# Kernel tuning notes

Measured on AMD Instinct MI355X. Metric: run time of the kernel, lower is better.

The kernel has to match this reference:

```python
import jax, jax.numpy as jnp
import numpy as np

N_CLASSES = 80
SEG_LEN = 512          # boxes per class (uniform segments)
H = 128                # hidden_size
DH = 2 * H             # decoder hidden (= concat of bidirectional encoder final hiddens)
EMB = 32               # decoder_input_dim
SOS, EOS = 2, 3


def _gru_cell(x, h, Wih, Whh, bih, bhh):
    # PyTorch GRU cell math. x:(in,), h:(hid,), Wih:(3*hid,in), Whh:(3*hid,hid)
    gi = Wih @ x + bih
    gh = Whh @ h + bhh
    i_r, i_z, i_n = jnp.split(gi, 3)
    h_r, h_z, h_n = jnp.split(gh, 3)
    r = jax.nn.sigmoid(i_r + h_r)
    z = jax.nn.sigmoid(i_z + h_z)
    n = jnp.tanh(i_n + r * h_n)
    return (1.0 - z) * n + z * h


def _gru_seq(xs, h0, Wih, Whh, bih, bhh):
    # xs: (T, in); returns final hidden (hid,) and all hiddens (T, hid)
    def step(h, x):
        h2 = _gru_cell(x, h, Wih, Whh, bih, bhh)
        return h2, h2
    hT, hs = jax.lax.scan(step, h0, xs)
    return hT, hs

# vmap over the 80 classes (per-class weights)
_run_gru = jax.vmap(_gru_seq, in_axes=(0, 0, 0, 0, 0, 0))


def setup_inputs() -> dict:
    key = jax.random.key(0)
    ks = jax.random.split(key, 32)
    N = N_CLASSES * SEG_LEN
    s = 0.05
    inp = {
        "feat": jax.random.normal(ks[0], (N, 1024), jnp.float32),
        "score": jax.random.uniform(ks[1], (N, 1), jnp.float32),
        "box": jax.random.uniform(ks[2], (N, 4), jnp.float32),
        "origin_score": jax.random.uniform(ks[3], (N, 91), jnp.float32),
        "labels": jax.random.randint(ks[4], (N,), 0, 2, jnp.int64),
        "weights": jax.random.uniform(ks[5], (N,), jnp.float32),
        "unique_class": jnp.ones((N_CLASSES,), jnp.int64),
        "unique_class_len": jnp.arange(N_CLASSES + 1, dtype=jnp.int64) * SEG_LEN,
        # shared linears
        "appear_W": jax.random.normal(ks[6], (H, 1024), jnp.float32) * s,
        "appear_b": jnp.zeros((H,), jnp.float32),
        "featlin_W": jax.random.normal(ks[7], (H, H + 96), jnp.float32) * s,
        "featlin_b": jnp.zeros((H,), jnp.float32),
        # per-class bidirectional encoder GRUs
        "enc_Wih_f": jax.random.normal(ks[8], (N_CLASSES, 3 * H, H), jnp.float32) * s,
        "enc_Whh_f": jax.random.normal(ks[9], (N_CLASSES, 3 * H, H), jnp.float32) * s,
        "enc_bih_f": jnp.zeros((N_CLASSES, 3 * H), jnp.float32),
        "enc_bhh_f": jnp.zeros((N_CLASSES, 3 * H), jnp.float32),
        "enc_Wih_b": jax.random.normal(ks[10], (N_CLASSES, 3 * H, H), jnp.float32) * s,
        "enc_Whh_b": jax.random.normal(ks[11], (N_CLASSES, 3 * H, H), jnp.float32) * s,
        "enc_bih_b": jnp.zeros((N_CLASSES, 3 * H), jnp.float32),
        "enc_bhh_b": jnp.zeros((N_CLASSES, 3 * H), jnp.float32),
        # decoder
        "dec_emb": jax.random.normal(ks[12], (4, EMB), jnp.float32) * s,
        "dec_Wih": jax.random.normal(ks[13], (N_CLASSES, 3 * DH, EMB), jnp.float32) * s,
        "dec_Whh": jax.random.normal(ks[14], (N_CLASSES, 3 * DH, DH), jnp.float32) * s,
        "dec_bih": jnp.zeros((N_CLASSES, 3 * DH), jnp.float32),
        "dec_bhh": jnp.zeros((N_CLASSES, 3 * DH), jnp.float32),
        "out_W": jax.random.normal(ks[15], (4, DH), jnp.float32) * s,
        "out_b": jnp.zeros((4,), jnp.float32),
    }
    return inp


def reference(feat, score, box, origin_score, labels, weights, unique_class,
              unique_class_len, appear_W, appear_b, featlin_W, featlin_b,
              enc_Wih_f, enc_Whh_f, enc_bih_f, enc_bhh_f,
              enc_Wih_b, enc_Whh_b, enc_bih_b, enc_bhh_b,
              dec_emb, dec_Wih, dec_Whh, dec_bih, dec_bhh, out_W, out_b):
    # --- shared feature encoding ---
    x = jax.nn.relu(feat @ appear_W.T + appear_b)                    # (N, H)
    allf = jnp.concatenate([x, score, box, origin_score], axis=1)    # (N, H+96)
    enc_feat = jax.nn.relu(allf @ featlin_W.T + featlin_b)           # (N, H)

    # --- per-class bidirectional encoder (uniform segments) ---
    seg = enc_feat.reshape(N_CLASSES, SEG_LEN, H)
    eos = jnp.ones((N_CLASSES, 1, H), enc_feat.dtype)                # encoder_EOS = ones
    enc_in = jnp.concatenate([seg, eos], axis=1)                     # (80, L+1, H)
    h0 = jnp.zeros((N_CLASSES, H), enc_feat.dtype)
    h_f, _ = _run_gru(enc_in, h0, enc_Wih_f, enc_Whh_f, enc_bih_f, enc_bhh_f)
    h_b, _ = _run_gru(enc_in[:, ::-1], h0, enc_Wih_b, enc_Whh_b, enc_bih_b, enc_bhh_b)
    dec_h0 = jnp.concatenate([h_f, h_b], axis=-1)                    # (80, 2H)

    # --- per-class decoder with teacher forcing (SOS then gold labels) ---
    emb = dec_emb[labels].reshape(N_CLASSES, SEG_LEN, EMB)
    sos = jnp.broadcast_to(dec_emb[SOS], (N_CLASSES, 1, EMB))
    dec_in = jnp.concatenate([sos, emb], axis=1)                     # (80, L+1, EMB)
    _, dec_hs = _run_gru(dec_in, dec_h0, dec_Wih, dec_Whh, dec_bih, dec_bhh)

    logits = dec_hs.reshape(-1, DH) @ out_W.T + out_b                # (80*(L+1), 4)
    output = jax.nn.log_softmax(logits, axis=-1)
    return output, labels, weights
```

## Files before the change

kernel.cpp:

```cpp
#include <hip/hip_runtime.h>


typedef __fp16 h2v __attribute__((ext_vector_type(2)));

__device__ __forceinline__ h2v pk2(float a, float b) {
  return __builtin_amdgcn_cvt_pkrtz(a, b);
}
__device__ __forceinline__ unsigned h2u(h2v h) { return __builtin_bit_cast(unsigned, h); }
__device__ __forceinline__ h2v u2h(unsigned u) { return __builtin_bit_cast(h2v, u); }
__device__ __forceinline__ float fdot2f(h2v a, h2v b, float c) {
  return __builtin_amdgcn_fdot2(a, b, c, false);
}
__device__ __forceinline__ float sigf(float x) { return 1.f / (1.f + __expf(-x)); }
__device__ __forceinline__ float tanhfast(float x) { return 2.f / (1.f + __expf(-2.f * x)) - 1.f; }

__device__ __forceinline__ uint4 pack8u(float4 a, float4 b) {
  uint4 o;
  o.x = h2u(pk2(a.x, a.y)); o.y = h2u(pk2(a.z, a.w));
  o.z = h2u(pk2(b.x, b.y)); o.w = h2u(pk2(b.z, b.w));
  return o;
}

__device__ __forceinline__ float dotu4(uint4 cv, h2v a0, h2v a1, h2v a2, h2v a3,
                                       float acc) {
  acc = fdot2f(u2h(cv.x), a0, acc);
  acc = fdot2f(u2h(cv.y), a1, acc);
  acc = fdot2f(u2h(cv.z), a2, acc);
  acc = fdot2f(u2h(cv.w), a3, acc);
  return acc;
}

template <int CTRL>
__device__ __forceinline__ float dppadd(float acc, float v) {
  int r = __builtin_amdgcn_update_dpp(0, __float_as_int(v), CTRL, 0xF, 0xF, true);
  return acc + __int_as_float(r);
}
__device__ __forceinline__ float swz4add(float acc, float v) {
  return acc + __int_as_float(__builtin_amdgcn_ds_swizzle(__float_as_int(v), 0x101F));
}

__device__ __forceinline__ float reduce8s(float p0, float p1, float p2, float p3,
                                          float p4, float p5, float p6, float p7) {
  p0 = dppadd<0xB1>(p0, p1);
  p2 = dppadd<0xB1>(p2, p3);
  p4 = dppadd<0xB1>(p4, p5);
  p6 = dppadd<0xB1>(p6, p7);
  p0 = dppadd<0x4E>(p0, p2);
  p4 = dppadd<0x4E>(p4, p6);
  p0 = swz4add(p0, p4);
  p0 = dppadd<0x128>(p0, p0);
  return p0;
}

#define BAR_LGKM()                                     \
  asm volatile("s_waitcnt lgkmcnt(0)" ::: "memory");   \
  __builtin_amdgcn_s_barrier();                        \
  asm volatile("" ::: "memory");

__global__ void k_fill_misc(const float* __restrict__ score, const float* __restrict__ box,
                            const float* __restrict__ orig, float* __restrict__ allf) {
  int i = blockIdx.x * blockDim.x + threadIdx.x;
  if (i >= 40960 * 96) return;
  int row = i / 96, k = i - row * 96;
  float v;
  if (k == 0) v = score[row];
  else if (k < 5) v = box[row * 4 + (k - 1)];
  else v = orig[(size_t)row * 91 + (k - 5)];
  allf[(size_t)row * 224 + 128 + k] = v;
}

__global__ __launch_bounds__(256) void k_gemm_appear(
    const float* __restrict__ A, const float* __restrict__ W,
    const float* __restrict__ bias, float* __restrict__ allf) {
  __shared__ float As[32][68];
  __shared__ float Ws[32][132];
  const int tid = threadIdx.x;
  const int tx = tid & 15, ty = tid >> 4;
  const int r0 = blockIdx.x * 64;
  const int lr = tid >> 3;
  const int lk = (tid & 7) * 4;
  float acc[4][8];
#pragma unroll
  for (int i = 0; i < 4; ++i)
#pragma unroll
    for (int j = 0; j < 8; ++j) acc[i][j] = 0.f;

  for (int k0 = 0; k0 < 1024; k0 += 32) {
#pragma unroll
    for (int i = 0; i < 2; ++i) {
      int rr = lr + i * 32;
      float4 v = *(const float4*)(A + (size_t)(r0 + rr) * 1024 + k0 + lk);
      As[lk + 0][rr] = v.x; As[lk + 1][rr] = v.y; As[lk + 2][rr] = v.z; As[lk + 3][rr] = v.w;
    }
#pragma unroll
    for (int i = 0; i < 4; ++i) {
      int wr = lr + i * 32;
      float4 v = *(const float4*)(W + (size_t)wr * 1024 + k0 + lk);
      Ws[lk + 0][wr] = v.x; Ws[lk + 1][wr] = v.y; Ws[lk + 2][wr] = v.z; Ws[lk + 3][wr] = v.w;
    }
    __syncthreads();
#pragma unroll
    for (int kk = 0; kk < 32; ++kk) {
      float4 a = *(const float4*)&As[kk][ty * 4];
      float4 w0 = *(const float4*)&Ws[kk][tx * 8];
      float4 w1 = *(const float4*)&Ws[kk][tx * 8 + 4];
      float av[4] = {a.x, a.y, a.z, a.w};
      float wv[8] = {w0.x, w0.y, w0.z, w0.w, w1.x, w1.y, w1.z, w1.w};
#pragma unroll
      for (int i = 0; i < 4; ++i)
#pragma unroll
        for (int j = 0; j < 8; ++j) acc[i][j] = fmaf(av[i], wv[j], acc[i][j]);
    }
    __syncthreads();
  }
#pragma unroll
  for (int i = 0; i < 4; ++i) {
    int row = r0 + ty * 4 + i;
#pragma unroll
    for (int j = 0; j < 8; ++j) {
      int col = tx * 8 + j;
      float v = acc[i][j] + bias[col];
      allf[(size_t)row * 224 + col] = fmaxf(v, 0.f);
    }
  }
}

__global__ __launch_bounds__(256) void k_gemm_featlin(
    const float* __restrict__ A, const float* __restrict__ W,
    const float* __restrict__ bias, unsigned* __restrict__ encf2) {
  __shared__ float As[32][68];
  __shared__ float Ws[32][132];
  const int tid = threadIdx.x;
  const int tx = tid & 15, ty = tid >> 4;
  const int r0 = blockIdx.x * 64;
  const int lr = tid >> 3;
  const int lk = (tid & 7) * 4;
  float acc[4][8];
#pragma unroll
  for (int i = 0; i < 4; ++i)
#pragma unroll
    for (int j = 0; j < 8; ++j) acc[i][j] = 0.f;

  for (int k0 = 0; k0 < 224; k0 += 32) {
#pragma unroll
    for (int i = 0; i < 2; ++i) {
      int rr = lr + i * 32;
      float4 v = *(const float4*)(A + (size_t)(r0 + rr) * 224 + k0 + lk);
      As[lk + 0][rr] = v.x; As[lk + 1][rr] = v.y; As[lk + 2][rr] = v.z; As[lk + 3][rr] = v.w;
    }
#pragma unroll
    for (int i = 0; i < 4; ++i) {
      int wr = lr + i * 32;
      float4 v = *(const float4*)(W + (size_t)wr * 224 + k0 + lk);
      Ws[lk + 0][wr] = v.x; Ws[lk + 1][wr] = v.y; Ws[lk + 2][wr] = v.z; Ws[lk + 3][wr] = v.w;
    }
    __syncthreads();
#pragma unroll
    for (int kk = 0; kk < 32; ++kk) {
      float4 a = *(const float4*)&As[kk][ty * 4];
      float4 w0 = *(const float4*)&Ws[kk][tx * 8];
      float4 w1 = *(const float4*)&Ws[kk][tx * 8 + 4];
      float av[4] = {a.x, a.y, a.z, a.w};
      float wv[8] = {w0.x, w0.y, w0.z, w0.w, w1.x, w1.y, w1.z, w1.w};
#pragma unroll
      for (int i = 0; i < 4; ++i)
#pragma unroll
        for (int j = 0; j < 8; ++j) acc[i][j] = fmaf(av[i], wv[j], acc[i][j]);
    }
    __syncthreads();
  }
#pragma unroll
  for (int i = 0; i < 4; ++i) {
    int row = r0 + ty * 4 + i;
    unsigned* orow = encf2 + (size_t)row * 64;
#pragma unroll
    for (int p = 0; p < 4; ++p) {
      int col = tx * 8 + 2 * p;
      float a = fmaxf(acc[i][2 * p] + bias[col], 0.f);
      float b = fmaxf(acc[i][2 * p + 1] + bias[col + 1], 0.f);
      orow[tx * 4 + p] = h2u(pk2(a, b));
    }
  }
}

__global__ __launch_bounds__(256) void k_dec_gi(
    const float* __restrict__ Wih, const float* __restrict__ bih,
    const float* __restrict__ emb, float* __restrict__ gi) {
  __shared__ float e[4][32];
  const int c = blockIdx.x, tid = threadIdx.x;
  if (tid < 128) e[tid >> 5][tid & 31] = emb[tid];
  __syncthreads();
#pragma unroll
  for (int i = 0; i < 3; ++i) {
    int r = tid + i * 256;
    const float* w = Wih + ((size_t)c * 768 + r) * 32;
    float b = bih[(size_t)c * 768 + r];
    float a0 = b, a1 = b, a2 = b, a3 = b;
#pragma unroll
    for (int k = 0; k < 32; ++k) {
      float wv = w[k];
      a0 = fmaf(wv, e[0][k], a0);
      a1 = fmaf(wv, e[1][k], a1);
      a2 = fmaf(wv, e[2][k], a2);
      a3 = fmaf(wv, e[3][k], a3);
    }
    gi[((size_t)c * 4 + 0) * 768 + r] = a0;
    gi[((size_t)c * 4 + 1) * 768 + r] = a1;
    gi[((size_t)c * 4 + 2) * 768 + r] = a2;
    gi[((size_t)c * 4 + 3) * 768 + r] = a3;
  }
}

__global__ __launch_bounds__(512) void k_pack_dec(
    const float* __restrict__ Whh, uint4* __restrict__ wpk) {
  const int c = blockIdx.x / 48, ic = blockIdx.x % 48;
  const int tid = threadIdx.x;
  const int G = tid >> 4, m = tid & 15, mw = m & 7;
  const int gt = ic >> 4, k = (ic & 15) >> 1, hf = ic & 1;
  const int row = gt * 256 + 8 * G + (k ^ mw);
  const float* src = Whh + ((size_t)c * 768 + row) * 256 + 16 * m + 8 * hf;
  wpk[((size_t)c * 48 + ic) * 512 + tid] =
      pack8u(*(const float4*)src, *(const float4*)(src + 4));
}

#define ELOAD(gt, k, DST)                                                          \
  {                                                                                \
    int rid_ = (k) ^ mw;                                                           \
    const float* Mx_ = ((k) & 1) ? baseB : baseA;                                  \
    const float4* ps_ =                                                            \
        (const float4*)(Mx_ + ((size_t)((gt) * 128 + 4 * G + (rid_ >> 1))) * 128 + \
                        8 * m);                                                    \
    DST = pack8u(ps_[0], ps_[1]);                                                  \
  }                                                                                \
  __builtin_amdgcn_sched_barrier(0);

__global__ __launch_bounds__(512) void k_enc_gru(
    const unsigned* __restrict__ encf2,
    const float* __restrict__ WihF, const float* __restrict__ WhhF,
    const float* __restrict__ bihF, const float* __restrict__ bhhF,
    const float* __restrict__ WihB, const float* __restrict__ WhhB,
    const float* __restrict__ bihB, const float* __restrict__ bhhB,
    float* __restrict__ dec_h0) {
  const int blk = blockIdx.x;
  const int c = blk >> 1, dir = blk & 1;
  const int tid = threadIdx.x;
  const int G = tid >> 4, m = tid & 15, mw = m & 7;

  const float* Wih = (dir ? WihB : WihF) + (size_t)c * 384 * 128;
  const float* Whh = (dir ? WhhB : WhhF) + (size_t)c * 384 * 128;
  const float* bih = (dir ? bihB : bihF) + (size_t)c * 384;
  const float* bhh = (dir ? bhhB : bhhF) + (size_t)c * 384;

  const float* baseA = (mw & 1) ? Whh : Wih;
  const float* baseB = (mw & 1) ? Wih : Whh;

  __shared__ __align__(16) unsigned x2s[2][64];
  __shared__ __align__(16) unsigned h2s[2][64];
  __shared__ __align__(16) uint4 wle[8 * 512];

  uint4 er0, er1, er2, er3, er4, er5, er6, er7;
  uint4 ez0, ez1, ez2, ez3, ez4, ez5, ez6, ez7;
  ELOAD(0, 0, er0) ELOAD(0, 1, er1) ELOAD(0, 2, er2) ELOAD(0, 3, er3)
  ELOAD(0, 4, er4) ELOAD(0, 5, er5) ELOAD(0, 6, er6) ELOAD(0, 7, er7)
  ELOAD(1, 0, ez0) ELOAD(1, 1, ez1) ELOAD(1, 2, ez2) ELOAD(1, 3, ez3)
  ELOAD(1, 4, ez4) ELOAD(1, 5, ez5) ELOAD(1, 6, ez6) ELOAD(1, 7, ez7)
  {
    uint4 t0;
    ELOAD(2, 0, t0) wle[0 * 512 + tid] = t0;
    ELOAD(2, 1, t0) wle[1 * 512 + tid] = t0;
    ELOAD(2, 2, t0) wle[2 * 512 + tid] = t0;
    ELOAD(2, 3, t0) wle[3 * 512 + tid] = t0;
    ELOAD(2, 4, t0) wle[4 * 512 + tid] = t0;
    ELOAD(2, 5, t0) wle[5 * 512 + tid] = t0;
    ELOAD(2, 6, t0) wle[6 * 512 + tid] = t0;
    ELOAD(2, 7, t0) wle[7 * 512 + tid] = t0;
  }

  const int u = 4 * G + (mw >> 1);
  const float brz_r = bih[u] + bhh[u];
  const float brz_z = bih[128 + u] + bhh[128 + u];
  const float b_in = bih[256 + u];
  const float b_hn = bhh[256 + u];

  if (tid < 64) h2s[0][tid] = 0u;
  if (tid >= 448) {
    int lane = tid - 448;
    x2s[0][lane] = (dir == 0) ? encf2[((size_t)c * 512 + 0) * 64 + lane] : 0x3C003C00u;
  }
  float hreg = 0.f;
  __syncthreads();

  const uint4* wl = wle + tid;

  for (int t = 0; t <= 512; ++t) {
    unsigned xpre = 0;
    if (tid >= 448 && t < 512) {
      int tn = t + 1, lane = tid - 448;
      int row = (dir == 0) ? ((tn < 512) ? tn : -1) : (512 - tn);
      xpre = (row < 0) ? 0x3C003C00u : encf2[((size_t)c * 512 + row) * 64 + lane];
    }
    uint4 xv = ((const uint4*)&x2s[t & 1][0])[m];
    uint4 hv = ((const uint4*)&h2s[t & 1][0])[m];
    h2v x0 = u2h(xv.x), x1 = u2h(xv.y), x2 = u2h(xv.z), x3 = u2h(xv.w);
    h2v hh0 = u2h(hv.x), hh1 = u2h(hv.y), hh2 = u2h(hv.z), hh3 = u2h(hv.w);
    bool oddl = (mw & 1);
    h2v a0 = oddl ? hh0 : x0, a1 = oddl ? hh1 : x1, a2 = oddl ? hh2 : x2, a3 = oddl ? hh3 : x3;
    h2v b0 = oddl ? x0 : hh0, b1 = oddl ? x1 : hh1, b2 = oddl ? x2 : hh2, b3 = oddl ? x3 : hh3;
#define EA(ch) dotu4(ch, a0, a1, a2, a3, 0.f)
#define EB(ch) dotu4(ch, b0, b1, b2, b3, 0.f)
    float vR = reduce8s(EA(er0), EB(er1), EA(er2), EB(er3),
                        EA(er4), EB(er5), EA(er6), EB(er7));
    float vZ = reduce8s(EA(ez0), EB(ez1), EA(ez2), EB(ez3),
                        EA(ez4), EB(ez5), EA(ez6), EB(ez7));
    float vN = reduce8s(EA(wl[0 * 512]), EB(wl[1 * 512]), EA(wl[2 * 512]), EB(wl[3 * 512]),
                        EA(wl[4 * 512]), EB(wl[5 * 512]), EA(wl[6 * 512]), EB(wl[7 * 512]));
#undef EA
#undef EB
    float oR = __shfl_xor(vR, 1, 64);
    float oZ = __shfl_xor(vZ, 1, 64);
    float oN = __shfl_xor(vN, 1, 64);
    float r = sigf(vR + oR + brz_r);
    float z = sigf(vZ + oZ + brz_z);
    float i_n = oddl ? oN : vN;
    float h_n = oddl ? vN : oN;
    float n = tanhfast(i_n + b_in + r * (h_n + b_hn));
    float hn = (1.f - z) * n + z * hreg;
    hreg = hn;
    float prt = __shfl_xor(hn, 2, 64);
    if (m < 8 && (mw & 3) == 0) h2s[(t + 1) & 1][2 * G + (mw >> 2)] = h2u(pk2(hn, prt));
    if (tid >= 448 && t < 512) x2s[(t + 1) & 1][tid - 448] = xpre;
    BAR_LGKM();
  }
  if ((m < 8) && ((mw & 1) == 0))
    dec_h0[(size_t)c * 256 + dir * 128 + u] = hreg;
}

#define CONSX(sa, sb) dotu4(sb, g4, g5, g6, g7, dotu4(sa, g0, g1, g2, g3, 0.f))

__global__ __launch_bounds__(512) void k_dec_gru(
    const uint4* __restrict__ wpk, const float* __restrict__ bhh,
    const float* __restrict__ gi, const float* __restrict__ h0,
    const int* __restrict__ labels, unsigned* __restrict__ dhs2) {
  const int c = blockIdx.x, tid = threadIdx.x;
  const int G = tid >> 4, m = tid & 15, mw = m & 7;

  __shared__ __align__(16) unsigned h2s[2][128];
  __shared__ int labs[513];
  __shared__ __align__(16) uint4 wlds[12 * 512];

  const uint4* wp = wpk + (size_t)c * 48 * 512 + tid;
  const uint4* wpS = wp + 36 * 512;

  for (int j = 0; j < 12; ++j) wlds[j * 512 + tid] = wp[(24 + j) * 512];
  __builtin_amdgcn_sched_barrier(0);
  uint4 ra0 = wp[0 * 512], ra1 = wp[1 * 512], ra2 = wp[2 * 512], ra3 = wp[3 * 512];
  uint4 ra4 = wp[4 * 512], ra5 = wp[5 * 512], ra6 = wp[6 * 512], ra7 = wp[7 * 512];
  __builtin_amdgcn_sched_barrier(0);
  uint4 ra8 = wp[8 * 512], ra9 = wp[9 * 512], ra10 = wp[10 * 512], ra11 = wp[11 * 512];
  uint4 ra12 = wp[12 * 512], ra13 = wp[13 * 512], ra14 = wp[14 * 512], ra15 = wp[15 * 512];
  __builtin_amdgcn_sched_barrier(0);
  uint4 ra16 = wp[16 * 512], ra17 = wp[17 * 512], ra18 = wp[18 * 512], ra19 = wp[19 * 512];
  uint4 ra20 = wp[20 * 512], ra21 = wp[21 * 512], ra22 = wp[22 * 512], ra23 = wp[23 * 512];
  __builtin_amdgcn_sched_barrier(0);
  uint4 ss0 = wpS[0 * 512], ss1 = wpS[1 * 512], ss2 = wpS[2 * 512], ss3 = wpS[3 * 512];
  uint4 ss4 = wpS[4 * 512], ss5 = wpS[5 * 512], ss6 = wpS[6 * 512], ss7 = wpS[7 * 512];
  uint4 ss8 = wpS[8 * 512], ss9 = wpS[9 * 512], ss10 = wpS[10 * 512], ss11 = wpS[11 * 512];

  const int u = 8 * G + mw;
  const float bb0 = bhh[(size_t)c * 768 + u];
  const float bb1 = bhh[(size_t)c * 768 + 256 + u];
  const float bb2 = bhh[(size_t)c * 768 + 512 + u];
  const float* gib = gi + (size_t)c * 4 * 768;
  unsigned* dout = dhs2 + (size_t)c * 513 * 128 + 4 * G + (mw >> 1);

  if (tid < 512) labs[tid + 1] = labels[(size_t)c * 512 + tid];
  if (tid == 0) labs[0] = 2;
  float hreg = h0[(size_t)c * 256 + u];
  {
    float oth = __shfl_xor(hreg, 1, 64);
    if (m < 8 && (mw & 1) == 0) h2s[0][4 * G + (mw >> 1)] = h2u(pk2(hreg, oth));
  }
  __syncthreads();

  const uint4* wl = wlds + tid;

  for (int t = 0; t <= 512; ++t) {
    uint4 ha = ((const uint4*)&h2s[t & 1][0])[2 * m];
    uint4 hb = ((const uint4*)&h2s[t & 1][0])[2 * m + 1];
    h2v g0 = u2h(ha.x), g1 = u2h(ha.y), g2 = u2h(ha.z), g3 = u2h(ha.w);
    h2v g4 = u2h(hb.x), g5 = u2h(hb.y), g6 = u2h(hb.z), g7 = u2h(hb.w);
    int sel = labs[t];
    const float* gp = gib + sel * 768;
    float giR = gp[u], giZ = gp[256 + u], giN = gp[512 + u];
    float p0 = CONSX(ra0, ra1), p1 = CONSX(ra2, ra3);
    float p2 = CONSX(ra4, ra5), p3 = CONSX(ra6, ra7);
    float p4 = CONSX(ra8, ra9), p5 = CONSX(ra10, ra11);
    float p6 = CONSX(ra12, ra13), p7 = CONSX(ra14, ra15);
    float rsum = reduce8s(p0, p1, p2, p3, p4, p5, p6, p7);
    p0 = CONSX(ra16, ra17); p1 = CONSX(ra18, ra19);
    p2 = CONSX(ra20, ra21); p3 = CONSX(ra22, ra23);
    p4 = CONSX(wl[0 * 512], wl[1 * 512]);
    p5 = CONSX(wl[2 * 512], wl[3 * 512]);
    p6 = CONSX(wl[4 * 512], wl[5 * 512]);
    p7 = CONSX(wl[6 * 512], wl[7 * 512]);
    float zsum = reduce8s(p0, p1, p2, p3, p4, p5, p6, p7);
    p0 = CONSX(wl[8 * 512], wl[9 * 512]);
    p1 = CONSX(wl[10 * 512], wl[11 * 512]);
    p2 = CONSX(ss0, ss1); ss0 = wpS[0 * 512]; ss1 = wpS[1 * 512];
    p3 = CONSX(ss2, ss3); ss2 = wpS[2 * 512]; ss3 = wpS[3 * 512];
    p4 = CONSX(ss4, ss5); ss4 = wpS[4 * 512]; ss5 = wpS[5 * 512];
    p5 = CONSX(ss6, ss7); ss6 = wpS[6 * 512]; ss7 = wpS[7 * 512];
    p6 = CONSX(ss8, ss9); ss8 = wpS[8 * 512]; ss9 = wpS[9 * 512];
    p7 = CONSX(ss10, ss11); ss10 = wpS[10 * 512]; ss11 = wpS[11 * 512];
    float nsum = reduce8s(p0, p1, p2, p3, p4, p5, p6, p7);
    float r = sigf(giR + rsum + bb0);
    float z = sigf(giZ + zsum + bb1);
    float n = tanhfast(giN + r * (nsum + bb2));
    float hn = (1.f - z) * n + z * hreg;
    hreg = hn;
    float oth = __shfl_xor(hn, 1, 64);
    if (m < 8 && (mw & 1) == 0) {
      unsigned pk = h2u(pk2(hn, oth));
      h2s[(t + 1) & 1][4 * G + (mw >> 1)] = pk;
      dout[(size_t)t * 128] = pk;
    }
    BAR_LGKM();
  }
}

__global__ __launch_bounds__(256) void k_out(
    const unsigned* __restrict__ dhs2, const float* __restrict__ outW,
    const float* __restrict__ outB, float* __restrict__ out) {
  int row = blockIdx.x * 4 + (threadIdx.x >> 6);
  if (row >= 41040) return;
  int lane = threadIdx.x & 63;
  const unsigned* hp = dhs2 + (size_t)row * 128 + 2 * lane;
  h2v ha = u2h(hp[0]), hb = u2h(hp[1]);
  float h0f = (float)ha[0], h1f = (float)ha[1], h2f = (float)hb[0], h3f = (float)hb[1];
  float p0, p1, p2, p3;
  {
    const float* w0 = outW + 4 * lane;
    const float* w1 = outW + 256 + 4 * lane;
    const float* w2 = outW + 512 + 4 * lane;
    const float* w3 = outW + 768 + 4 * lane;
    p0 = h0f * w0[0] + h1f * w0[1] + h2f * w0[2] + h3f * w0[3];
    p1 = h0f * w1[0] + h1f * w1[1] + h2f * w1[2] + h3f * w1[3];
    p2 = h0f * w2[0] + h1f * w2[1] + h2f * w2[2] + h3f * w2[3];
    p3 = h0f * w3[0] + h1f * w3[1] + h2f * w3[2] + h3f * w3[3];
  }
#pragma unroll
  for (int off = 32; off > 0; off >>= 1) {
    p0 += __shfl_xor(p0, off, 64);
    p1 += __shfl_xor(p1, off, 64);
    p2 += __shfl_xor(p2, off, 64);
    p3 += __shfl_xor(p3, off, 64);
  }
  if (lane == 0) {
    float l0 = p0 + outB[0], l1 = p1 + outB[1], l2 = p2 + outB[2], l3 = p3 + outB[3];
    float mm = fmaxf(fmaxf(l0, l1), fmaxf(l2, l3));
    float s = __expf(l0 - mm) + __expf(l1 - mm) + __expf(l2 - mm) + __expf(l3 - mm);
    float lse = mm + __logf(s);
    float* o = out + (size_t)row * 4;
    o[0] = l0 - lse; o[1] = l1 - lse; o[2] = l2 - lse; o[3] = l3 - lse;
  }
}

__global__ void k_passthrough(const int* __restrict__ labels,
                              const float* __restrict__ weights,
                              float* __restrict__ out) {
  int i = blockIdx.x * blockDim.x + threadIdx.x;
  if (i < 40960) {
    out[164160 + i] = (float)labels[i];
    out[164160 + 40960 + i] = weights[i];
  }
}

extern "C" void kernel_launch(void* const* d_in, const int* in_sizes, int n_in,
                              void* d_out, int out_size, void* d_ws, size_t ws_size,
                              hipStream_t stream) {
  (void)in_sizes; (void)n_in; (void)out_size; (void)ws_size;
  const float* feat = (const float*)d_in[0];
  const float* score = (const float*)d_in[1];
  const float* box = (const float*)d_in[2];
  const float* orig = (const float*)d_in[3];
  const int* labels = (const int*)d_in[4];
  const float* weights = (const float*)d_in[5];
  const float* appear_W = (const float*)d_in[8];
  const float* appear_b = (const float*)d_in[9];
  const float* featlin_W = (const float*)d_in[10];
  const float* featlin_b = (const float*)d_in[11];
  const float* eWihF = (const float*)d_in[12];
  const float* eWhhF = (const float*)d_in[13];
  const float* ebihF = (const float*)d_in[14];
  const float* ebhhF = (const float*)d_in[15];
  const float* eWihB = (const float*)d_in[16];
  const float* eWhhB = (const float*)d_in[17];
  const float* ebihB = (const float*)d_in[18];
  const float* ebhhB = (const float*)d_in[19];
  const float* dec_emb = (const float*)d_in[20];
  const float* dWih = (const float*)d_in[21];
  const float* dWhh = (const float*)d_in[22];
  const float* dbih = (const float*)d_in[23];
  const float* dbhh = (const float*)d_in[24];
  const float* outW = (const float*)d_in[25];
  const float* outB = (const float*)d_in[26];
  float* out = (float*)d_out;

  char* ws = (char*)d_ws;
  float* allf = (float*)ws;
  unsigned* encf2 = (unsigned*)(ws + (size_t)40960 * 224 * 4);
  float* dec_h0 = (float*)(ws + (size_t)40960 * 224 * 4 + (size_t)40960 * 64 * 4);
  float* dec_gi = dec_h0 + 80 * 256;
  unsigned* dhs2 = (unsigned*)(dec_gi + 80 * 4 * 768);
  uint4* wpack = (uint4*)allf;

  k_fill_misc<<<15360, 256, 0, stream>>>(score, box, orig, allf);
  k_gemm_appear<<<640, 256, 0, stream>>>(feat, appear_W, appear_b, allf);
  k_gemm_featlin<<<640, 256, 0, stream>>>(allf, featlin_W, featlin_b, encf2);
  k_pack_dec<<<80 * 48, 512, 0, stream>>>(dWhh, wpack);
  k_dec_gi<<<80, 256, 0, stream>>>(dWih, dbih, dec_emb, dec_gi);
  k_enc_gru<<<160, 512, 0, stream>>>(encf2, eWihF, eWhhF, ebihF, ebhhF,
                                     eWihB, eWhhB, ebihB, ebhhB, dec_h0);
  k_dec_gru<<<80, 512, 0, stream>>>(wpack, dbhh, dec_gi, dec_h0, labels, dhs2);
  k_out<<<10260, 256, 0, stream>>>(dhs2, outW, outB, out);
  k_passthrough<<<160, 256, 0, stream>>>(labels, weights, out);
}
```

Measured before the change: 1.557 ms.

## Split decoder GRU rows across thread pairs with 1024-thread blocks

The decoder GRU kernel now runs 1024 threads per block instead of 512. Each hidden unit's dot product over its K dimension is split between two adjacent lanes, which combine their partial sums with a lane shuffle. The weight packing kernel is reorganised to match this layout. Per-thread register-held and LDS-held weight chunks are roughly halved, which shortens the serial per-step dot-product chain. In exchange it adds an extra shuffle reduction and a larger barrier across 16 waves per step.

```diff
diff --git a/kernel.cpp b/kernel.cpp
--- a/kernel.cpp
+++ b/kernel.cpp
@@ -211,15 +211,17 @@
   }
 }
 
-__global__ __launch_bounds__(512) void k_pack_dec(
+__global__ __launch_bounds__(1024) void k_pack_dec(
     const float* __restrict__ Whh, uint4* __restrict__ wpk) {
-  const int c = blockIdx.x / 48, ic = blockIdx.x % 48;
+  const int c = blockIdx.x / 24, ic = blockIdx.x % 24;
   const int tid = threadIdx.x;
   const int G = tid >> 4, m = tid & 15, mw = m & 7;
-  const int gt = ic >> 4, k = (ic & 15) >> 1, hf = ic & 1;
-  const int row = gt * 256 + 8 * G + (k ^ mw);
+  const int gt = ic >> 3, k = ic & 7;
+  const int rid = k ^ mw;
+  const int row = gt * 256 + 4 * G + (rid >> 1);
+  const int hf = rid & 1;
   const float* src = Whh + ((size_t)c * 768 + row) * 256 + 16 * m + 8 * hf;
-  wpk[((size_t)c * 48 + ic) * 512 + tid] =
+  wpk[((size_t)c * 24 + ic) * 1024 + tid] =
       pack8u(*(const float4*)src, *(const float4*)(src + 4));
 }
 
@@ -335,9 +337,7 @@
     dec_h0[(size_t)c * 256 + dir * 128 + u] = hreg;
 }
 
-#define CONSX(sa, sb) dotu4(sb, g4, g5, g6, g7, dotu4(sa, g0, g1, g2, g3, 0.f))
-
-__global__ __launch_bounds__(512) void k_dec_gru(
+__global__ __launch_bounds__(1024) void k_dec_gru(
     const uint4* __restrict__ wpk, const float* __restrict__ bhh,
     const float* __restrict__ gi, const float* __restrict__ h0,
     const int* __restrict__ labels, unsigned* __restrict__ dhs2) {
@@ -346,39 +346,33 @@
 
   __shared__ __align__(16) unsigned h2s[2][128];
   __shared__ int labs[513];
-  __shared__ __align__(16) uint4 wlds[12 * 512];
-
-  const uint4* wp = wpk + (size_t)c * 48 * 512 + tid;
-  const uint4* wpS = wp + 36 * 512;
-
-  for (int j = 0; j < 12; ++j) wlds[j * 512 + tid] = wp[(24 + j) * 512];
+  __shared__ __align__(16) uint4 wlds[9 * 1024];
+
+  const uint4* wp = wpk + (size_t)c * 24 * 1024 + tid;
+  const uint4* wpS = wp + 21 * 1024;
+
+  for (int j = 0; j < 9; ++j) wlds[j * 1024 + tid] = wp[(12 + j) * 1024];
   __builtin_amdgcn_sched_barrier(0);
-  uint4 ra0 = wp[0 * 512], ra1 = wp[1 * 512], ra2 = wp[2 * 512], ra3 = wp[3 * 512];
-  uint4 ra4 = wp[4 * 512], ra5 = wp[5 * 512], ra6 = wp[6 * 512], ra7 = wp[7 * 512];
+  uint4 rr0 = wp[0 * 1024], rr1 = wp[1 * 1024], rr2 = wp[2 * 1024], rr3 = wp[3 * 1024];
+  uint4 rr4 = wp[4 * 1024], rr5 = wp[5 * 1024], rr6 = wp[6 * 1024], rr7 = wp[7 * 1024];
   __builtin_amdgcn_sched_barrier(0);
-  uint4 ra8 = wp[8 * 512], ra9 = wp[9 * 512], ra10 = wp[10 * 512], ra11 = wp[11 * 512];
-  uint4 ra12 = wp[12 * 512], ra13 = wp[13 * 512], ra14 = wp[14 * 512], ra15 = wp[15 * 512];
+  uint4 rz0 = wp[8 * 1024], rz1 = wp[9 * 1024], rz2 = wp[10 * 1024], rz3 = wp[11 * 1024];
   __builtin_amdgcn_sched_barrier(0);
-  uint4 ra16 = wp[16 * 512], ra17 = wp[17 * 512], ra18 = wp[18 * 512], ra19 = wp[19 * 512];
-  uint4 ra20 = wp[20 * 512], ra21 = wp[21 * 512], ra22 = wp[22 * 512], ra23 = wp[23 * 512];
-  __builtin_amdgcn_sched_barrier(0);
-  uint4 ss0 = wpS[0 * 512], ss1 = wpS[1 * 512], ss2 = wpS[2 * 512], ss3 = wpS[3 * 512];
-  uint4 ss4 = wpS[4 * 512], ss5 = wpS[5 * 512], ss6 = wpS[6 * 512], ss7 = wpS[7 * 512];
-  uint4 ss8 = wpS[8 * 512], ss9 = wpS[9 * 512], ss10 = wpS[10 * 512], ss11 = wpS[11 * 512];
-
-  const int u = 8 * G + mw;
-  const float bb0 = bhh[(size_t)c * 768 + u];
-  const float bb1 = bhh[(size_t)c * 768 + 256 + u];
-  const float bb2 = bhh[(size_t)c * 768 + 512 + u];
+  uint4 ss0 = wpS[0 * 1024], ss1 = wpS[1 * 1024], ss2 = wpS[2 * 1024];
+
+  const int u = 4 * G + (mw >> 1);
+  const float bbR = bhh[(size_t)c * 768 + u];
+  const float bbZ = bhh[(size_t)c * 768 + 256 + u];
+  const float bbN = bhh[(size_t)c * 768 + 512 + u];
   const float* gib = gi + (size_t)c * 4 * 768;
-  unsigned* dout = dhs2 + (size_t)c * 513 * 128 + 4 * G + (mw >> 1);
+  unsigned* dout = dhs2 + (size_t)c * 513 * 128 + 2 * G + (mw >> 2);
 
   if (tid < 512) labs[tid + 1] = labels[(size_t)c * 512 + tid];
   if (tid == 0) labs[0] = 2;
   float hreg = h0[(size_t)c * 256 + u];
   {
-    float oth = __shfl_xor(hreg, 1, 64);
-    if (m < 8 && (mw & 1) == 0) h2s[0][4 * G + (mw >> 1)] = h2u(pk2(hreg, oth));
+    float oth = __shfl_xor(hreg, 2, 64);
+    if (m < 8 && (mw & 3) == 0) h2s[0][2 * G + (mw >> 2)] = h2u(pk2(hreg, oth));
   }
   __syncthreads();
 
@@ -389,39 +383,42 @@
     uint4 hb = ((const uint4*)&h2s[t & 1][0])[2 * m + 1];
     h2v g0 = u2h(ha.x), g1 = u2h(ha.y), g2 = u2h(ha.z), g3 = u2h(ha.w);
     h2v g4 = u2h(hb.x), g5 = u2h(hb.y), g6 = u2h(hb.z), g7 = u2h(hb.w);
+    bool oddl = (mw & 1);
+    h2v ga0 = oddl ? g4 : g0, ga1 = oddl ? g5 : g1, ga2 = oddl ? g6 : g2, ga3 = oddl ? g7 : g3;
+    h2v gb0 = oddl ? g0 : g4, gb1 = oddl ? g1 : g5, gb2 = oddl ? g2 : g6, gb3 = oddl ? g3 : g7;
+#define CA(ch) dotu4(ch, ga0, ga1, ga2, ga3, 0.f)
+#define CB(ch) dotu4(ch, gb0, gb1, gb2, gb3, 0.f)
     int sel = labs[t];
     const float* gp = gib + sel * 768;
     float giR = gp[u], giZ = gp[256 + u], giN = gp[512 + u];
-    float p0 = CONSX(ra0, ra1), p1 = CONSX(ra2, ra3);
-    float p2 = CONSX(ra4, ra5), p3 = CONSX(ra6, ra7);
-    float p4 = CONSX(ra8, ra9), p5 = CONSX(ra10, ra11);
-    float p6 = CONSX(ra12, ra13), p7 = CONSX(ra14, ra15);
-    float rsum = reduce8s(p0, p1, p2, p3, p4, p5, p6, p7);
-    p0 = CONSX(ra16, ra17); p1 = CONSX(ra18, ra19);
-    p2 = CONSX(ra20, ra21); p3 = CONSX(ra22, ra23);
-    p4 = CONSX(wl[0 * 512], wl[1 * 512]);
-    p5 = CONSX(wl[2 * 512], wl[3 * 512]);
-    p6 = CONSX(wl[4 * 512], wl[5 * 512]);
-    p7 = CONSX(wl[6 * 512], wl[7 * 512]);
-    float zsum = reduce8s(p0, p1, p2, p3, p4, p5, p6, p7);
-    p0 = CONSX(wl[8 * 512], wl[9 * 512]);
-    p1 = CONSX(wl[10 * 512], wl[11 * 512]);
-    p2 = CONSX(ss0, ss1); ss0 = wpS[0 * 512]; ss1 = wpS[1 * 512];
-    p3 = CONSX(ss2, ss3); ss2 = wpS[2 * 512]; ss3 = wpS[3 * 512];
-    p4 = CONSX(ss4, ss5); ss4 = wpS[4 * 512]; ss5 = wpS[5 * 512];
-    p5 = CONSX(ss6, ss7); ss6 = wpS[6 * 512]; ss7 = wpS[7 * 512];
-    p6 = CONSX(ss8, ss9); ss8 = wpS[8 * 512]; ss9 = wpS[9 * 512];
-    p7 = CONSX(ss10, ss11); ss10 = wpS[10 * 512]; ss11 = wpS[11 * 512];
-    float nsum = reduce8s(p0, p1, p2, p3, p4, p5, p6, p7);
-    float r = sigf(giR + rsum + bb0);
-    float z = sigf(giZ + zsum + bb1);
-    float n = tanhfast(giN + r * (nsum + bb2));
+    float vR = reduce8s(CA(rr0), CB(rr1), CA(rr2), CB(rr3),
+                        CA(rr4), CB(rr5), CA(rr6), CB(rr7));
+    float vZ = reduce8s(CA(rz0), CB(rz1), CA(rz2), CB(rz3),
+                        CA(wl[0 * 1024]), CB(wl[1 * 1024]),
+                        CA(wl[2 * 1024]), CB(wl[3 * 1024]));
+    float p0 = CA(wl[4 * 1024]);
+    float p1 = CB(wl[5 * 1024]);
+    float p2 = CA(wl[6 * 1024]);
+    float p3 = CB(wl[7 * 1024]);
+    float p4 = CA(wl[8 * 1024]);
+    float p5 = CB(ss0); ss0 = wpS[0 * 1024];
+    float p6 = CA(ss1); ss1 = wpS[1 * 1024];
+    float p7 = CB(ss2); ss2 = wpS[2 * 1024];
+    float vN = reduce8s(p0, p1, p2, p3, p4, p5, p6, p7);
+#undef CA
+#undef CB
+    float rsum = vR + __shfl_xor(vR, 1, 64);
+    float zsum = vZ + __shfl_xor(vZ, 1, 64);
+    float nsum = vN + __shfl_xor(vN, 1, 64);
+    float r = sigf(giR + rsum + bbR);
+    float z = sigf(giZ + zsum + bbZ);
+    float n = tanhfast(giN + r * (nsum + bbN));
     float hn = (1.f - z) * n + z * hreg;
     hreg = hn;
-    float oth = __shfl_xor(hn, 1, 64);
-    if (m < 8 && (mw & 1) == 0) {
+    float oth = __shfl_xor(hn, 2, 64);
+    if (m < 8 && (mw & 3) == 0) {
       unsigned pk = h2u(pk2(hn, oth));
-      h2s[(t + 1) & 1][4 * G + (mw >> 1)] = pk;
+      h2s[(t + 1) & 1][2 * G + (mw >> 2)] = pk;
       dout[(size_t)t * 128] = pk;
     }
     BAR_LGKM();
@@ -517,11 +514,11 @@
   k_fill_misc<<<15360, 256, 0, stream>>>(score, box, orig, allf);
   k_gemm_appear<<<640, 256, 0, stream>>>(feat, appear_W, appear_b, allf);
   k_gemm_featlin<<<640, 256, 0, stream>>>(allf, featlin_W, featlin_b, encf2);
-  k_pack_dec<<<80 * 48, 512, 0, stream>>>(dWhh, wpack);
+  k_pack_dec<<<80 * 24, 1024, 0, stream>>>(dWhh, wpack);
   k_dec_gi<<<80, 256, 0, stream>>>(dWih, dbih, dec_emb, dec_gi);
   k_enc_gru<<<160, 512, 0, stream>>>(encf2, eWihF, eWhhF, ebihF, ebhhF,
                                      eWihB, eWhhB, ebihB, ebhhB, dec_h0);
-  k_dec_gru<<<80, 512, 0, stream>>>(wpack, dbhh, dec_gi, dec_h0, labels, dhs2);
+  k_dec_gru<<<80, 1024, 0, stream>>>(wpack, dbhh, dec_gi, dec_h0, labels, dhs2);
   k_out<<<10260, 256, 0, stream>>>(dhs2, outW, outB, out);
   k_passthrough<<<160, 256, 0, stream>>>(labels, weights, out);
 }
```

Measured after the change: 1.752 ms. 12.5% more time.

## Rebalance decoder GRU weight residency: fewer registers, more LDS, streamed global

Applied to the files above, without the earlier changes.

Decoder GRU weights were split across registers (24 uint4), LDS (12 uint4) and a register-prefetched global stream (12 uint4). They are now split 12 in registers, 18 in LDS and 18 reloaded from global (L1/L2) every timestep inside the loop. This lowers register pressure but adds per-step cache traffic and LDS reads on the serial critical path, where global load latency may be exposed.

```diff
diff --git a/kernel.cpp b/kernel.cpp
--- a/kernel.cpp
+++ b/kernel.cpp
@@ -346,25 +346,17 @@
 
   __shared__ __align__(16) unsigned h2s[2][128];
   __shared__ int labs[513];
-  __shared__ __align__(16) uint4 wlds[12 * 512];
+  __shared__ __align__(16) uint4 wlds[18 * 512];
 
   const uint4* wp = wpk + (size_t)c * 48 * 512 + tid;
-  const uint4* wpS = wp + 36 * 512;
-
-  for (int j = 0; j < 12; ++j) wlds[j * 512 + tid] = wp[(24 + j) * 512];
+
+  for (int j = 0; j < 18; ++j) wlds[j * 512 + tid] = wp[(12 + j) * 512];
   __builtin_amdgcn_sched_barrier(0);
   uint4 ra0 = wp[0 * 512], ra1 = wp[1 * 512], ra2 = wp[2 * 512], ra3 = wp[3 * 512];
   uint4 ra4 = wp[4 * 512], ra5 = wp[5 * 512], ra6 = wp[6 * 512], ra7 = wp[7 * 512];
   __builtin_amdgcn_sched_barrier(0);
   uint4 ra8 = wp[8 * 512], ra9 = wp[9 * 512], ra10 = wp[10 * 512], ra11 = wp[11 * 512];
-  uint4 ra12 = wp[12 * 512], ra13 = wp[13 * 512], ra14 = wp[14 * 512], ra15 = wp[15 * 512];
   __builtin_amdgcn_sched_barrier(0);
-  uint4 ra16 = wp[16 * 512], ra17 = wp[17 * 512], ra18 = wp[18 * 512], ra19 = wp[19 * 512];
-  uint4 ra20 = wp[20 * 512], ra21 = wp[21 * 512], ra22 = wp[22 * 512], ra23 = wp[23 * 512];
-  __builtin_amdgcn_sched_barrier(0);
-  uint4 ss0 = wpS[0 * 512], ss1 = wpS[1 * 512], ss2 = wpS[2 * 512], ss3 = wpS[3 * 512];
-  uint4 ss4 = wpS[4 * 512], ss5 = wpS[5 * 512], ss6 = wpS[6 * 512], ss7 = wpS[7 * 512];
-  uint4 ss8 = wpS[8 * 512], ss9 = wpS[9 * 512], ss10 = wpS[10 * 512], ss11 = wpS[11 * 512];
 
   const int u = 8 * G + mw;
   const float bb0 = bhh[(size_t)c * 768 + u];
@@ -385,6 +377,8 @@
   const uint4* wl = wlds + tid;
 
   for (int t = 0; t <= 512; ++t) {
+    uint4 sa0 = wp[30 * 512], sa1 = wp[31 * 512], sa2 = wp[32 * 512], sa3 = wp[33 * 512];
+    uint4 sa4 = wp[34 * 512], sa5 = wp[35 * 512], sa6 = wp[36 * 512], sa7 = wp[37 * 512];
     uint4 ha = ((const uint4*)&h2s[t & 1][0])[2 * m];
     uint4 hb = ((const uint4*)&h2s[t & 1][0])[2 * m + 1];
     h2v g0 = u2h(ha.x), g1 = u2h(ha.y), g2 = u2h(ha.z), g3 = u2h(ha.w);
@@ -395,23 +389,29 @@
     float p0 = CONSX(ra0, ra1), p1 = CONSX(ra2, ra3);
     float p2 = CONSX(ra4, ra5), p3 = CONSX(ra6, ra7);
     float p4 = CONSX(ra8, ra9), p5 = CONSX(ra10, ra11);
-    float p6 = CONSX(ra12, ra13), p7 = CONSX(ra14, ra15);
+    float p6 = CONSX(wl[0 * 512], wl[1 * 512]);
+    float p7 = CONSX(wl[2 * 512], wl[3 * 512]);
     float rsum = reduce8s(p0, p1, p2, p3, p4, p5, p6, p7);
-    p0 = CONSX(ra16, ra17); p1 = CONSX(ra18, ra19);
-    p2 = CONSX(ra20, ra21); p3 = CONSX(ra22, ra23);
-    p4 = CONSX(wl[0 * 512], wl[1 * 512]);
-    p5 = CONSX(wl[2 * 512], wl[3 * 512]);
-    p6 = CONSX(wl[4 * 512], wl[5 * 512]);
-    p7 = CONSX(wl[6 * 512], wl[7 * 512]);
+    uint4 sb0 = wp[38 * 512], sb1 = wp[39 * 512], sb2 = wp[40 * 512], sb3 = wp[41 * 512];
+    uint4 sb4 = wp[42 * 512], sb5 = wp[43 * 512], sb6 = wp[44 * 512], sb7 = wp[45 * 512];
+    uint4 sb8 = wp[46 * 512], sb9 = wp[47 * 512];
+    p0 = CONSX(wl[4 * 512], wl[5 * 512]);
+    p1 = CONSX(wl[6 * 512], wl[7 * 512]);
+    p2 = CONSX(wl[8 * 512], wl[9 * 512]);
+    p3 = CONSX(wl[10 * 512], wl[11 * 512]);
+    p4 = CONSX(wl[12 * 512], wl[13 * 512]);
+    p5 = CONSX(wl[14 * 512], wl[15 * 512]);
+    p6 = CONSX(wl[16 * 512], wl[17 * 512]);
+    p7 = CONSX(sa0, sa1);
     float zsum = reduce8s(p0, p1, p2, p3, p4, p5, p6, p7);
-    p0 = CONSX(wl[8 * 512], wl[9 * 512]);
-    p1 = CONSX(wl[10 * 512], wl[11 * 512]);
-    p2 = CONSX(ss0, ss1); ss0 = wpS[0 * 512]; ss1 = wpS[1 * 512];
-    p3 = CONSX(ss2, ss3); ss2 = wpS[2 * 512]; ss3 = wpS[3 * 512];
-    p4 = CONSX(ss4, ss5); ss4 = wpS[4 * 512]; ss5 = wpS[5 * 512];
-    p5 = CONSX(ss6, ss7); ss6 = wpS[6 * 512]; ss7 = wpS[7 * 512];
-    p6 = CONSX(ss8, ss9); ss8 = wpS[8 * 512]; ss9 = wpS[9 * 512];
-    p7 = CONSX(ss10, ss11); ss10 = wpS[10 * 512]; ss11 = wpS[11 * 512];
+    p0 = CONSX(sa2, sa3);
+    p1 = CONSX(sa4, sa5);
+    p2 = CONSX(sa6, sa7);
+    p3 = CONSX(sb0, sb1);
+    p4 = CONSX(sb2, sb3);
+    p5 = CONSX(sb4, sb5);
+    p6 = CONSX(sb6, sb7);
+    p7 = CONSX(sb8, sb9);
     float nsum = reduce8s(p0, p1, p2, p3, p4, p5, p6, p7);
     float r = sigf(giR + rsum + bb0);
     float z = sigf(giZ + zsum + bb1);
```

Measured after the change: 1.552 ms. Within noise of the previous version (-0.3%).
